# Kernel tuning notes

Measured on AMD Instinct MI355X. Metric: run time of the kernel, lower is better.

## Reference

```python
import jax, jax.numpy as jnp
import numpy as np

B, N, E, ITERS = 8, 1024, 10, 5


def _xavier(key, shape):
    fan_in, fan_out = shape[1], shape[0]
    std = float(np.sqrt(2.0 / (fan_in + fan_out)))
    return jax.random.normal(key, shape, dtype=jnp.float32) * std


def setup_inputs() -> dict:
    key = jax.random.key(0)
    ks = jax.random.split(key, 10)
    return {
        "features": jax.random.uniform(ks[0], (B, N), dtype=jnp.float32),
        "weights": jax.random.uniform(ks[1], (B, N, N), dtype=jnp.float32),
        "adjacency": jax.random.uniform(ks[2], (B, N, N), dtype=jnp.float32),
        # torch Linear(in, out) weight has shape (out, in); y = x @ W.T
        "w_selected": _xavier(ks[3], (E, 1)),
        "w_nbpriors": _xavier(ks[4], (E, E)),
        "w_nbweights": _xavier(ks[5], (E, E)),
        "w_nbweights_ew": _xavier(ks[6], (E, 1)),
        "w_q_reduc": _xavier(ks[7], (1, 2 * E)),
        "w_q_allembed": _xavier(ks[8], (E, E)),
        "w_q_action": _xavier(ks[9], (E, E)),
    }


def reference(features, weights, adjacency, w_selected, w_nbpriors,
              w_nbweights, w_nbweights_ew, w_q_reduc, w_q_allembed, w_q_action):
    b, n = features.shape
    e = w_selected.shape[0]
    # v_selected = Linear(1,E)(features[...,None]) -> outer product with (E,) vector
    v_selected = features[:, :, None] * w_selected[:, 0]            # [B,N,E]
    # relu(Linear(1,E)(weights[...,None])), then sum over dim=1 (source nodes)
    w_exp = jax.nn.relu(weights[:, :, :, None] * w_nbweights_ew[:, 0])  # [B,N,N,E]
    v_weights = jnp.einsum('bje,fe->bjf', jnp.sum(w_exp, axis=1), w_nbweights)  # [B,N,E]
    base = v_selected + v_weights

    embeddings = jnp.zeros((b, n, e), dtype=features.dtype)
    for _ in range(ITERS):
        v_priors = jnp.einsum('bij,bje->bie', adjacency, embeddings)  # [B,N,E]
        v_priors = jnp.einsum('bie,fe->bif', v_priors, w_nbpriors)
        embeddings = jax.nn.relu(base + v_priors)

    sumembed = jnp.einsum('bne,fe->bf', embeddings, w_q_allembed)     # [B,E]
    sumembed = jnp.broadcast_to(sumembed[:, None, :], (b, n, e))
    peract = jnp.einsum('bne,fe->bnf', embeddings, w_q_action)        # [B,N,E]
    q_in = jnp.concatenate([sumembed, peract], axis=2)                # [B,N,2E]
    q_vals = jnp.einsum('bnk,ok->bno', q_in, w_q_reduc)[:, :, 0]      # [B,N]
    return q_vals, embeddings
```

## Files before the change

### kernel.cpp

```cpp
#include <hip/hip_runtime.h>

#define B 8
#define N 1024
#define E 10
#define GP 44
#define EMB_FLOATS (256 * GP)
#define EMB_F4 (EMB_FLOATS / 4)
#define NBLK 256
#define TPB 32
#define BAR_PAD 32

typedef float f32x4 __attribute__((ext_vector_type(4)));

__device__ __forceinline__ void batch_barrier(unsigned* cnt) {
    __syncthreads();
    if (threadIdx.x == 0) {
        __hip_atomic_fetch_add(cnt, 1u, __ATOMIC_RELAXED, __HIP_MEMORY_SCOPE_AGENT);
        while (__hip_atomic_load(cnt, __ATOMIC_RELAXED, __HIP_MEMORY_SCOPE_AGENT) < TPB)
            __builtin_amdgcn_s_sleep(2);
    }
    __syncthreads();
    asm volatile("" ::: "memory");
}

__device__ __forceinline__ void store_llc(float* p, float v) {
    __hip_atomic_store((unsigned*)p, __float_as_uint(v),
                       __ATOMIC_RELAXED, __HIP_MEMORY_SCOPE_AGENT);
}
__device__ __forceinline__ float load_llc(const float* p) {
    unsigned u = __hip_atomic_load((const unsigned*)p,
                                   __ATOMIC_RELAXED, __HIP_MEMORY_SCOPE_AGENT);
    return __uint_as_float(u);
}

__global__ __launch_bounds__(1024, 4) void k_fused(
    const float* __restrict__ W, const float* __restrict__ features,
    const float* __restrict__ w_sel, const float* __restrict__ w_nbw,
    const float* __restrict__ w_ew, const float* __restrict__ A,
    const float* __restrict__ Wp, const float* __restrict__ w_reduc,
    const float* __restrict__ w_all, const float* __restrict__ w_act,
    float* eA, float* eB,
    float* __restrict__ emb_out, float* __restrict__ qv,
    float* __restrict__ qpart, unsigned* __restrict__ bars)
{
    __shared__ float4 EmS[EMB_F4];
    __shared__ float vred[16][9][2 * E];
    __shared__ float WpS[E * E];
    __shared__ float gaS[E], gactS[E];
    __shared__ float vS[32 * E], qS[32 * E], qrow[32];
    __shared__ float qsumS;

    int bx = blockIdx.x, tid = threadIdx.x;
    int b = bx >> 5, tile = bx & 31;
    int i0 = tile * 32;
    int m = tid >> 6;
    int s = tid & 63;
    unsigned* mybars = bars + b * BAR_PAD;

    float Arf[2][4][4];
    {
        const float* Ab = A + ((size_t)(b * N) + i0 + m) * N + 4 * s;
#pragma unroll
        for (int k = 0; k < 2; ++k)
#pragma unroll
            for (int c = 0; c < 4; ++c) {
                float4 t = *(const float4*)(Ab + (size_t)(16 * k) * N + 256 * c);
                Arf[k][c][0] = t.x; Arf[k][c][1] = t.y;
                Arf[k][c][2] = t.z; Arf[k][c][3] = t.w;
            }
    }

    if (tid < E * E) WpS[tid] = Wp[tid];
    if (tid < E) {
        float sa = 0.f, sc = 0.f;
#pragma unroll
        for (int k = 0; k < E; ++k) {
            sa += w_reduc[k] * w_all[k * E + tid];
            sc += w_reduc[E + k] * w_act[k * E + tid];
        }
        gaS[tid] = sa;
        gactS[tid] = sc;
    }

    float b_reg = 0.f;
    {
        float* redPt = (float*)&EmS[0];
        float* redNt = redPt + 32 * 129;
        float* scol  = redNt + 32 * 129;
        int c4 = (tid & 7) * 4;
        int rg = tid >> 3;
        const float* wp = W + ((size_t)b * N + rg * 8) * N + i0 + c4;
        float4 sp = {0.f, 0.f, 0.f, 0.f}, sn = {0.f, 0.f, 0.f, 0.f};
#pragma unroll
        for (int i = 0; i < 8; ++i) {
            float4 w = *(const float4*)(wp + (size_t)i * N);
            sp.x += fmaxf(w.x, 0.f); sn.x += fmaxf(-w.x, 0.f);
            sp.y += fmaxf(w.y, 0.f); sn.y += fmaxf(-w.y, 0.f);
            sp.z += fmaxf(w.z, 0.f); sn.z += fmaxf(-w.z, 0.f);
            sp.w += fmaxf(w.w, 0.f); sn.w += fmaxf(-w.w, 0.f);
        }
        redPt[(c4 + 0) * 129 + rg] = sp.x; redNt[(c4 + 0) * 129 + rg] = sn.x;
        redPt[(c4 + 1) * 129 + rg] = sp.y; redNt[(c4 + 1) * 129 + rg] = sn.y;
        redPt[(c4 + 2) * 129 + rg] = sp.z; redNt[(c4 + 2) * 129 + rg] = sn.z;
        redPt[(c4 + 3) * 129 + rg] = sp.w; redNt[(c4 + 3) * 129 + rg] = sn.w;
        __syncthreads();
        if (tid < 64) {
            int cc = tid & 31;
            const float* rp = (tid < 32) ? redPt : redNt;
            float t = 0.f;
#pragma unroll 8
            for (int g = 0; g < 128; ++g) t += rp[cc * 129 + g];
            scol[(tid >> 5) * 32 + cc] = t;
        }
        __syncthreads();
        if (tid < 32 * E) {
            int cc = tid / E, f = tid % E;
            float spc = scol[cc], snc = scol[32 + cc];
            float acc = features[(b << 10) + i0 + cc] * w_sel[f];
#pragma unroll
            for (int e = 0; e < E; ++e) {
                float ce = w_ew[e];
                float se = (ce > 0.f) ? ce * spc : (-ce) * snc;
                acc += w_nbw[f * E + e] * se;
            }
            b_reg = acc;
            int row = i0 + cc;
            store_llc(&eA[(size_t)b * EMB_FLOATS + (row >> 2) * GP + (row & 3) * E + f],
                      fmaxf(acc, 0.f));
        }
    }
    batch_barrier(&mybars[0]);

    float da = 0.f;
    for (int it = 0; it < 4; ++it) {
        const float* ein = (it & 1) ? (const float*)eB : (const float*)eA;
        float* eout = (it & 1) ? eA : eB;

        {
            const f32x4* src = (const f32x4*)ein + (size_t)b * EMB_F4;
            f32x4 t0, t1, t2 = {0.f, 0.f, 0.f, 0.f};
            asm volatile("global_load_dwordx4 %0, %1, off sc0 sc1"
                         : "=v"(t0) : "v"(src + tid) : "memory");
            asm volatile("global_load_dwordx4 %0, %1, off sc0 sc1"
                         : "=v"(t1) : "v"(src + tid + 1024) : "memory");
            if (tid < EMB_F4 - 2048)
                asm volatile("global_load_dwordx4 %0, %1, off sc0 sc1"
                             : "=v"(t2) : "v"(src + tid + 2048) : "memory");
            asm volatile("s_waitcnt vmcnt(0)" ::: "memory");
            __builtin_amdgcn_sched_barrier(0);
            ((f32x4*)EmS)[tid]        = t0;
            ((f32x4*)EmS)[tid + 1024] = t1;
            if (tid < EMB_F4 - 2048) ((f32x4*)EmS)[tid + 2048] = t2;
        }
        __syncthreads();

        float acc[2][E];
#pragma unroll
        for (int k = 0; k < 2; ++k)
#pragma unroll
            for (int e = 0; e < E; ++e) acc[k][e] = 0.f;

#pragma unroll
        for (int c = 0; c < 4; ++c) {
            float4 g4[10];
            const float4* gp = EmS + (size_t)(s + 64 * c) * (GP / 4);
#pragma unroll
            for (int t = 0; t < 10; ++t) g4[t] = gp[t];
            const float* g40 = (const float*)g4;
#pragma unroll
            for (int q = 0; q < 4; ++q)
#pragma unroll
                for (int k = 0; k < 2; ++k) {
                    float a = Arf[k][c][q];
#pragma unroll
                    for (int e = 0; e < E; ++e)
                        acc[k][e] += a * g40[q * E + e];
                }
        }

#pragma unroll
        for (int mask = 1; mask <= 4; mask <<= 1)
#pragma unroll
            for (int k = 0; k < 2; ++k)
#pragma unroll
                for (int e = 0; e < E; ++e)
                    acc[k][e] += __shfl_xor(acc[k][e], mask, 64);
        if ((s & 7) == 0)
#pragma unroll
            for (int k = 0; k < 2; ++k)
#pragma unroll
                for (int e = 0; e < E; ++e)
                    vred[m][s >> 3][k * E + e] = acc[k][e];
        __syncthreads();

        if (tid < 32 * E) {
            int r = tid / E, f = tid % E;
            int mm = r & 15, kk = r >> 4;
            float v[E];
#pragma unroll
            for (int e = 0; e < E; ++e) {
                float t = 0.f;
#pragma unroll
                for (int g = 0; g < 8; ++g) t += vred[mm][g][kk * E + e];
                v[e] = t;
            }
            float d = 0.f;
#pragma unroll
            for (int e = 0; e < E; ++e) d += v[e] * WpS[f * E + e];
            float r_out = fmaxf(b_reg + d, 0.f);
            if (it < 3) {
                int grow = i0 + r;
                store_llc(&eout[(size_t)b * EMB_FLOATS + (grow >> 2) * GP + (grow & 3) * E + f],
                          r_out);
            } else {
                size_t gi = (size_t)((b << 10) + i0 + r);
                emb_out[gi * E + f] = r_out;
                vS[tid] = r_out * gactS[f];
                qS[tid] = r_out * gaS[f];
            }
        }
        if (it < 3) batch_barrier(&mybars[(1 + it) * B * BAR_PAD]);
    }

    __syncthreads();
    if (tid < 32) {
        float dg = 0.f;
#pragma unroll
        for (int f = 0; f < E; ++f) {
            da += vS[tid * E + f];
            dg += qS[tid * E + f];
        }
        qrow[tid] = dg;
    }
    __syncthreads();
    if (tid == 0) {
        float t = 0.f;
#pragma unroll
        for (int r = 0; r < 32; ++r) t += qrow[r];
        store_llc(&qpart[bx], t);
    }
    batch_barrier(&mybars[4 * B * BAR_PAD]);

    if (tid < 32) {
        float t = load_llc(&qpart[(b << 5) + tid]);
#pragma unroll
        for (int mask = 1; mask < 32; mask <<= 1)
            t += __shfl_xor(t, mask, 32);
        if (tid == 0) qsumS = t;
    }
    __syncthreads();
    if (tid < 32) qv[(b << 10) + i0 + tid] = da + qsumS;
}

extern "C" void kernel_launch(void* const* d_in, const int* in_sizes, int n_in,
                              void* d_out, int out_size, void* d_ws, size_t ws_size,
                              hipStream_t stream) {
    const float* features  = (const float*)d_in[0];
    const float* W         = (const float*)d_in[1];
    const float* adjacency = (const float*)d_in[2];
    const float* w_sel     = (const float*)d_in[3];
    const float* w_pri     = (const float*)d_in[4];
    const float* w_nbw     = (const float*)d_in[5];
    const float* w_ew      = (const float*)d_in[6];
    const float* w_reduc   = (const float*)d_in[7];
    const float* w_all     = (const float*)d_in[8];
    const float* w_act     = (const float*)d_in[9];

    float* out     = (float*)d_out;
    float* qv      = out;
    float* emb_out = out + B * N;

    float* ws      = (float*)d_ws;
    float* eA      = ws;
    float* eB      = eA + (size_t)B * EMB_FLOATS;
    float* qpart   = eB + (size_t)B * EMB_FLOATS;
    unsigned* bars = (unsigned*)(qpart + NBLK);

    hipMemsetAsync(bars, 0, 5 * B * BAR_PAD * sizeof(unsigned), stream);
    k_fused<<<NBLK, 1024, 0, stream>>>(W, features, w_sel, w_nbw, w_ew,
                                       adjacency, w_pri, w_reduc, w_all, w_act,
                                       eA, eB, emb_out, qv, qpart, bars);
}
```

Before: 147.8 us.

## Retile adjacency matvec so each thread handles four rows over two column chunks

Changes the thread-to-work mapping of the A·emb product: each thread now keeps a 4-row × 2-chunk slice of adjacency in registers instead of 2 rows × 4 chunks. Each embedding fetch from shared memory is therefore reused across four rows, which halves LDS reads per FMA. The embedding loads are split into two halves to reduce register pressure. The cost is more accumulators and one extra shuffle-reduction stage, and the partial-sum reduction layout is reworked to match.

```diff
diff --git a/kernel.cpp b/kernel.cpp
--- a/kernel.cpp
+++ b/kernel.cpp
@@ -44,7 +44,7 @@
     float* __restrict__ qpart, unsigned* __restrict__ bars)
 {
     __shared__ float4 EmS[EMB_F4];
-    __shared__ float vred[16][9][2 * E];
+    __shared__ float vred[16][5][4 * E];
     __shared__ float WpS[E * E];
     __shared__ float gaS[E], gactS[E];
     __shared__ float vS[32 * E], qS[32 * E], qrow[32];
@@ -53,20 +53,22 @@
     int bx = blockIdx.x, tid = threadIdx.x;
     int b = bx >> 5, tile = bx & 31;
     int i0 = tile * 32;
-    int m = tid >> 6;
+    int w = tid >> 6;
     int s = tid & 63;
+    int rs = tid >> 7;
+    int jg = tid & 127;
     unsigned* mybars = bars + b * BAR_PAD;
 
-    float Arf[2][4][4];
+    float Arf[4][2][4];
     {
-        const float* Ab = A + ((size_t)(b * N) + i0 + m) * N + 4 * s;
-#pragma unroll
-        for (int k = 0; k < 2; ++k)
-#pragma unroll
-            for (int c = 0; c < 4; ++c) {
-                float4 t = *(const float4*)(Ab + (size_t)(16 * k) * N + 256 * c);
-                Arf[k][c][0] = t.x; Arf[k][c][1] = t.y;
-                Arf[k][c][2] = t.z; Arf[k][c][3] = t.w;
+        const float* Ab = A + ((size_t)(b * N) + i0 + (rs << 2)) * N + 4 * jg;
+#pragma unroll
+        for (int rr = 0; rr < 4; ++rr)
+#pragma unroll
+            for (int c = 0; c < 2; ++c) {
+                float4 t = *(const float4*)(Ab + (size_t)rr * N + 512 * c);
+                Arf[rr][c][0] = t.x; Arf[rr][c][1] = t.y;
+                Arf[rr][c][2] = t.z; Arf[rr][c][3] = t.w;
             }
     }
 
@@ -93,11 +95,11 @@
         float4 sp = {0.f, 0.f, 0.f, 0.f}, sn = {0.f, 0.f, 0.f, 0.f};
 #pragma unroll
         for (int i = 0; i < 8; ++i) {
-            float4 w = *(const float4*)(wp + (size_t)i * N);
-            sp.x += fmaxf(w.x, 0.f); sn.x += fmaxf(-w.x, 0.f);
-            sp.y += fmaxf(w.y, 0.f); sn.y += fmaxf(-w.y, 0.f);
-            sp.z += fmaxf(w.z, 0.f); sn.z += fmaxf(-w.z, 0.f);
-            sp.w += fmaxf(w.w, 0.f); sn.w += fmaxf(-w.w, 0.f);
+            float4 ww = *(const float4*)(wp + (size_t)i * N);
+            sp.x += fmaxf(ww.x, 0.f); sn.x += fmaxf(-ww.x, 0.f);
+            sp.y += fmaxf(ww.y, 0.f); sn.y += fmaxf(-ww.y, 0.f);
+            sp.z += fmaxf(ww.z, 0.f); sn.z += fmaxf(-ww.z, 0.f);
+            sp.w += fmaxf(ww.w, 0.f); sn.w += fmaxf(-ww.w, 0.f);
         }
         redPt[(c4 + 0) * 129 + rg] = sp.x; redNt[(c4 + 0) * 129 + rg] = sn.x;
         redPt[(c4 + 1) * 129 + rg] = sp.y; redNt[(c4 + 1) * 129 + rg] = sn.y;
@@ -154,54 +156,74 @@
         }
         __syncthreads();
 
-        float acc[2][E];
-#pragma unroll
-        for (int k = 0; k < 2; ++k)
-#pragma unroll
-            for (int e = 0; e < E; ++e) acc[k][e] = 0.f;
-
-#pragma unroll
-        for (int c = 0; c < 4; ++c) {
-            float4 g4[10];
-            const float4* gp = EmS + (size_t)(s + 64 * c) * (GP / 4);
-#pragma unroll
-            for (int t = 0; t < 10; ++t) g4[t] = gp[t];
-            const float* g40 = (const float*)g4;
-#pragma unroll
-            for (int q = 0; q < 4; ++q)
-#pragma unroll
-                for (int k = 0; k < 2; ++k) {
-                    float a = Arf[k][c][q];
-#pragma unroll
-                    for (int e = 0; e < E; ++e)
-                        acc[k][e] += a * g40[q * E + e];
-                }
-        }
-
-#pragma unroll
-        for (int mask = 1; mask <= 4; mask <<= 1)
-#pragma unroll
-            for (int k = 0; k < 2; ++k)
+        float acc[4][E];
+#pragma unroll
+        for (int rr = 0; rr < 4; ++rr)
+#pragma unroll
+            for (int e = 0; e < E; ++e) acc[rr][e] = 0.f;
+
+#pragma unroll
+        for (int c = 0; c < 2; ++c) {
+            const float4* gp = EmS + (size_t)(jg + 128 * c) * (GP / 4);
+            {
+                float4 g4a[5];
+#pragma unroll
+                for (int t = 0; t < 5; ++t) g4a[t] = gp[t];
+                const float* ga = (const float*)g4a;
+#pragma unroll
+                for (int q = 0; q < 2; ++q)
+#pragma unroll
+                    for (int rr = 0; rr < 4; ++rr) {
+                        float a = Arf[rr][c][q];
+#pragma unroll
+                        for (int e = 0; e < E; ++e)
+                            acc[rr][e] += a * ga[q * E + e];
+                    }
+            }
+            {
+                float4 g4b[5];
+#pragma unroll
+                for (int t = 0; t < 5; ++t) g4b[t] = gp[5 + t];
+                const float* gb = (const float*)g4b;
+#pragma unroll
+                for (int q = 0; q < 2; ++q)
+#pragma unroll
+                    for (int rr = 0; rr < 4; ++rr) {
+                        float a = Arf[rr][c][q + 2];
+#pragma unroll
+                        for (int e = 0; e < E; ++e)
+                            acc[rr][e] += a * gb[q * E + e];
+                    }
+            }
+        }
+
+#pragma unroll
+        for (int mask = 1; mask <= 8; mask <<= 1)
+#pragma unroll
+            for (int rr = 0; rr < 4; ++rr)
 #pragma unroll
                 for (int e = 0; e < E; ++e)
-                    acc[k][e] += __shfl_xor(acc[k][e], mask, 64);
-        if ((s & 7) == 0)
-#pragma unroll
-            for (int k = 0; k < 2; ++k)
+                    acc[rr][e] += __shfl_xor(acc[rr][e], mask, 64);
+        if ((s & 15) == 0)
+#pragma unroll
+            for (int rr = 0; rr < 4; ++rr)
 #pragma unroll
                 for (int e = 0; e < E; ++e)
-                    vred[m][s >> 3][k * E + e] = acc[k][e];
+                    vred[w][s >> 4][rr * E + e] = acc[rr][e];
         __syncthreads();
 
         if (tid < 32 * E) {
             int r = tid / E, f = tid % E;
-            int mm = r & 15, kk = r >> 4;
+            int prs = r >> 2, rr = r & 3;
             float v[E];
 #pragma unroll
             for (int e = 0; e < E; ++e) {
                 float t = 0.f;
 #pragma unroll
-                for (int g = 0; g < 8; ++g) t += vred[mm][g][kk * E + e];
+                for (int h = 0; h < 2; ++h)
+#pragma unroll
+                    for (int p = 0; p < 4; ++p)
+                        t += vred[(prs << 1) + h][p][rr * E + e];
                 v[e] = t;
             }
             float d = 0.f;
```

Result: slower. 228.3 us (+54.4%).
